# Optimization experiments

Measured on AMD Instinct MI355X. Metric: run time of the kernel, lower is better.

## Reference

```python
import jax, jax.numpy as jnp
import numpy as np

N_NODES = 20000
N_EDGES = 320000
H = 4        # heads
C = 64       # channels per head
D = H * C    # 256, also input_dim
L = 4        # num_layers
NEG_SLOPE = 0.2


def setup_inputs() -> dict:
    key = jax.random.key(0)
    ks = jax.random.split(key, 8)
    x = jax.random.normal(ks[0], (N_NODES, D), jnp.float32)
    edge_index = jax.random.randint(ks[1], (2, N_EDGES), 0, N_NODES, dtype=jnp.int64)
    Ws = jax.random.normal(ks[2], (L, D, D), jnp.float32) * 0.05
    att_src = jax.random.normal(ks[3], (L, H, C), jnp.float32) * 0.05
    att_dst = jax.random.normal(ks[4], (L, H, C), jnp.float32) * 0.05
    biases = jax.random.normal(ks[5], (L, D), jnp.float32) * 0.05
    Wout = jax.random.normal(ks[6], (D, D), jnp.float32) * 0.05
    bout = jax.random.normal(ks[7], (D,), jnp.float32) * 0.05
    return {"x": x, "edge_index": edge_index, "Ws": Ws, "att_src": att_src,
            "att_dst": att_dst, "biases": biases, "Wout": Wout, "bout": bout}


def reference(x, edge_index, Ws, att_src, att_dst, biases, Wout, bout):
    n = x.shape[0]
    # PyG GATConv adds self-loops by default; same edge set each layer.
    loops = jnp.arange(n, dtype=edge_index.dtype)
    src = jnp.concatenate([edge_index[0], loops])  # message sources
    dst = jnp.concatenate([edge_index[1], loops])  # message targets (softmax groups)
    h = x
    for l in range(L):
        hp = (h @ Ws[l]).reshape(n, H, C)                      # [N,H,C]
        a_s = jnp.einsum('nhc,hc->nh', hp, att_src[l])          # [N,H]
        a_d = jnp.einsum('nhc,hc->nh', hp, att_dst[l])          # [N,H]
        e = jax.nn.leaky_relu(a_s[src] + a_d[dst], NEG_SLOPE)   # [E',H]
        # per-destination segment softmax (every node has a self-loop -> non-empty)
        m = jax.ops.segment_max(e, dst, num_segments=n)         # [N,H]
        ex = jnp.exp(e - m[dst])
        denom = jax.ops.segment_sum(ex, dst, num_segments=n)    # [N,H]
        alpha = ex / denom[dst]                                 # [E',H]
        msg = hp[src] * alpha[:, :, None]                       # [E',H,C]
        h = jax.ops.segment_sum(msg, dst, num_segments=n).reshape(n, D) + biases[l]
        h = jax.nn.elu(h)  # dropout is identity in eval mode
    g = jnp.mean(h, axis=0, keepdims=True)                      # mean pooling, single graph
    return g @ Wout + bout                                      # [1, D]
```

## Files before the change

### kernel.cpp

```cpp
#include <hip/hip_runtime.h>
#include <hip/hip_bf16.h>

#define H 4
#define C 64
#define D 256
#define NEG_SLOPE 0.2f
#define ESHIFT 8.0f

typedef _Float16 half_t;
typedef __attribute__((ext_vector_type(8))) _Float16 half8v;
typedef __attribute__((ext_vector_type(4))) float f32x4;


__device__ inline void fma_mix_pair(float& clo, float& chi, unsigned wu, float a) {
    asm("v_fma_mix_f32 %0, %2, %3, %0 op_sel_hi:[1,0,0]\n\t"
        "v_fma_mix_f32 %1, %2, %3, %1 op_sel:[1,0,0] op_sel_hi:[1,0,0]"
        : "+v"(clo), "+v"(chi)
        : "v"(wu), "v"(a));
}

__global__ void count_kernel(const int* __restrict__ ei, int E, int N, int* __restrict__ counts) {
    int i = blockIdx.x * blockDim.x + threadIdx.x;
    if (i >= E + N) return;
    int d = (i < E) ? ei[E + i] : (i - E);
    atomicAdd(&counts[d], 1);
}

__global__ __launch_bounds__(1024) void scan1(const int* __restrict__ counts,
                                              int* __restrict__ row_ptr,
                                              int* __restrict__ bsum, int N) {
    __shared__ int wsum[16];
    int tid = threadIdx.x, lane = tid & 63, wid = tid >> 6;
    int idx = blockIdx.x * 1024 + tid;
    int v = (idx < N) ? counts[idx] : 0;
    int val = v;
    #pragma unroll
    for (int o = 1; o < 64; o <<= 1) {
        int t = __shfl_up(val, o);
        if (lane >= o) val += t;
    }
    if (lane == 63) wsum[wid] = val;
    __syncthreads();
    int woff = 0;
    #pragma unroll
    for (int w = 0; w < 16; w++) woff += (w < wid) ? wsum[w] : 0;
    if (idx < N) row_ptr[idx] = woff + val - v;
    if (tid == 1023) bsum[blockIdx.x] = woff + val;
}

__global__ void scan2(int* __restrict__ bsum, int* __restrict__ row_ptr, int nb, int N) {
    int lane = threadIdx.x;
    int v = (lane < nb) ? bsum[lane] : 0;
    int val = v;
    #pragma unroll
    for (int o = 1; o < 64; o <<= 1) {
        int t = __shfl_up(val, o);
        if (lane >= o) val += t;
    }
    if (lane < nb) bsum[lane] = val - v;
    if (lane == 63) row_ptr[N] = val;
}

__global__ __launch_bounds__(1024) void scan3(int* __restrict__ row_ptr,
                                              const int* __restrict__ bsum,
                                              int* __restrict__ cursor, int N) {
    int idx = blockIdx.x * 1024 + threadIdx.x;
    if (idx >= N) return;
    int r = row_ptr[idx] + bsum[blockIdx.x];
    row_ptr[idx] = r;
    cursor[idx] = r;
}

__global__ void scatter_kernel(const int* __restrict__ ei, int E, int N,
                               int* __restrict__ cursor, int* __restrict__ csr_src) {
    int i = blockIdx.x * blockDim.x + threadIdx.x;
    if (i >= E + N) return;
    int s, d;
    if (i < E) { s = ei[i]; d = ei[E + i]; }
    else       { s = d = i - E; }
    int pos = atomicAdd(&cursor[d], 1);
    csr_src[pos] = s;
}

__global__ void conv_x(const float* __restrict__ in, half_t* __restrict__ xt, int total) {
    int t = blockIdx.x * blockDim.x + threadIdx.x;
    if (t >= total) return;
    int i = t >> 5, o = t & 31;
    const float* src = in + (size_t)i * 256 + o * 8;
    float4 v0 = *(const float4*)src;
    float4 v1 = *(const float4*)(src + 4);
    half_t q[8] __attribute__((aligned(16)));
    q[0] = (half_t)v0.x; q[1] = (half_t)v0.y; q[2] = (half_t)v0.z; q[3] = (half_t)v0.w;
    q[4] = (half_t)v1.x; q[5] = (half_t)v1.y; q[6] = (half_t)v1.z; q[7] = (half_t)v1.w;
    size_t dst = (size_t)(i >> 4) * 4096 + (o >> 2) * 512 + (o & 3) * 128 + (i & 15) * 8;
    *(half8v*)(xt + dst) = *(half8v*)q;
}

__global__ void conv_w(const float* __restrict__ W, half_t* __restrict__ wt, int total) {
    int idx = blockIdx.x * blockDim.x + threadIdx.x;
    if (idx >= total) return;
    int Lr = idx & 63;
    int s  = (idx >> 6) & 7;
    int cb = (idx >> 9) & 3;
    int h  = (idx >> 11) & 3;
    int l  = idx >> 13;
    int col = h * 64 + cb * 16 + (Lr & 15);
    int k0  = 32 * s + (Lr >> 4) * 8;
    half_t q[8] __attribute__((aligned(16)));
    #pragma unroll
    for (int j = 0; j < 8; j++)
        q[j] = (half_t)W[(size_t)l * 65536 + (size_t)(k0 + j) * 256 + col];
    *(half8v*)(wt + (size_t)idx * 8) = *(half8v*)q;
}

__global__ __launch_bounds__(256) void gemm_f16(
    const half_t* __restrict__ At, const half_t* __restrict__ Wt,
    const float* __restrict__ asrc, const float* __restrict__ adst,
    half_t* __restrict__ hp, float* __restrict__ as_out, float* __restrict__ ad_out,
    int Npad) {
    __shared__ float sp[2][4][16], sd[2][4][16];
    int cb = threadIdx.x >> 6, lane = threadIdx.x & 63;
    int h = blockIdx.x & 3, pg = blockIdx.x >> 2;
    int rlo = lane & 15, q = lane >> 4;
    const half_t* pb = Wt + (size_t)h * 16384 + (size_t)cb * 4096 + lane * 8;

    half8v B[8];
    #pragma unroll
    for (int s = 0; s < 8; s++) B[s] = *(const half8v*)(pb + s * 512);

    float av = asrc[h * 64 + cb * 16 + rlo];
    float dv = adst[h * 64 + cb * 16 + rlo];
    half_t* hph = hp + (size_t)h * Npad * 64;

    #pragma unroll
    for (int pp = 0; pp < 4; pp++) {
        int p = pg * 4 + pp;
        const half_t* pa = At + (size_t)p * 4096 + lane * 8;

        f32x4 acc = (f32x4){0.f, 0.f, 0.f, 0.f};
        half8v A0 = *(const half8v*)(pa);
        half8v A1;
        #pragma unroll
        for (int s = 0; s < 8; s += 2) {
            A1 = *(const half8v*)(pa + (s + 1) * 512);
            acc = __builtin_amdgcn_mfma_f32_16x16x32_f16(A0, B[s], acc, 0, 0, 0);
            if (s < 6) A0 = *(const half8v*)(pa + (s + 2) * 512);
            acc = __builtin_amdgcn_mfma_f32_16x16x32_f16(A1, B[s + 1], acc, 0, 0, 0);
        }

        int grow = p * 16 + q * 4;
        #pragma unroll
        for (int i = 0; i < 4; i++)
            hph[(size_t)(grow + i) * 64 + cb * 16 + rlo] = (half_t)acc[i];

        float ps[4], pd[4];
        #pragma unroll
        for (int i = 0; i < 4; i++) { ps[i] = acc[i] * av; pd[i] = acc[i] * dv; }
        #pragma unroll
        for (int mask = 1; mask <= 8; mask <<= 1) {
            #pragma unroll
            for (int i = 0; i < 4; i++) {
                ps[i] += __shfl_xor(ps[i], mask);
                pd[i] += __shfl_xor(pd[i], mask);
            }
        }
        int par = pp & 1;
        if (rlo == 0) {
            #pragma unroll
            for (int i = 0; i < 4; i++) {
                sp[par][cb][q * 4 + i] = ps[i];
                sd[par][cb][q * 4 + i] = pd[i];
            }
        }
        __syncthreads();
        if (threadIdx.x < 16) {
            int r = threadIdx.x;
            float s_ = sp[par][0][r] + sp[par][1][r] + sp[par][2][r] + sp[par][3][r];
            float d_ = sd[par][0][r] + sd[par][1][r] + sd[par][2][r] + sd[par][3][r];
            as_out[(size_t)(p * 16 + r) * 4 + h] = s_;
            ad_out[(size_t)(p * 16 + r) * 4 + h] = d_;
        }
    }
}

#define AGG_BODY(g)                                                          \
    {                                                                        \
        int e_ = 2 * (g) + es;                                               \
        int s_ = __float_as_int(pk[wv][e_][0]);                              \
        float a_ = pk[wv][e_][4 + hh];                                       \
        const uint4 w_ = *(const uint4*)(hpb + (size_t)s_ * 64);             \
        asum += a_;                                                          \
        fma_mix_pair(c0, c1, w_.x, a_);                                      \
        fma_mix_pair(c2, c3, w_.y, a_);                                      \
        fma_mix_pair(c4, c5, w_.z, a_);                                      \
        fma_mix_pair(c6, c7, w_.w, a_);                                      \
    }

__global__ __launch_bounds__(256) void gat_aggregate(
    const half_t* __restrict__ hp, const float* __restrict__ as_, const float* __restrict__ ad_,
    const int* __restrict__ row_ptr, const int* __restrict__ csr_src,
    const float* __restrict__ bias, half_t* __restrict__ hnext, int N, int Npad) {
    __shared__ float pk[4][64][8];
    int wv = threadIdx.x >> 6, lane = threadIdx.x & 63;
    int d = blockIdx.x * 4 + wv;
    if (d >= N) return;
    int r0 = row_ptr[d], deg = row_ptr[d + 1] - r0;
    float4 adv = *(const float4*)&ad_[(size_t)d * 4];

    if (deg <= 64) {
        if (lane < deg) {
            int s = csr_src[r0 + lane];
            float4 as4 = *(const float4*)&as_[(size_t)s * 4];
            float e0 = as4.x + adv.x, e1 = as4.y + adv.y;
            float e2 = as4.z + adv.z, e3 = as4.w + adv.w;
            e0 = e0 > 0.f ? e0 : NEG_SLOPE * e0;
            e1 = e1 > 0.f ? e1 : NEG_SLOPE * e1;
            e2 = e2 > 0.f ? e2 : NEG_SLOPE * e2;
            e3 = e3 > 0.f ? e3 : NEG_SLOPE * e3;
            float4 ex;
            ex.x = __expf(e0 - ESHIFT);
            ex.y = __expf(e1 - ESHIFT);
            ex.z = __expf(e2 - ESHIFT);
            ex.w = __expf(e3 - ESHIFT);
            pk[wv][lane][0] = __int_as_float(s);
            *(float4*)&pk[wv][lane][4] = ex;
        }

        int hh = lane >> 4;
        int es = (lane >> 3) & 1;
        int chq = lane & 7;
        const half_t* hpb = hp + (size_t)hh * Npad * 64 + chq * 8;
        float c0 = 0.f, c1 = 0.f, c2 = 0.f, c3 = 0.f;
        float c4 = 0.f, c5 = 0.f, c6 = 0.f, c7 = 0.f;
        float asum = 0.f;
        int full = deg >> 1;
        int g = 0;
        for (; g + 4 <= full; g += 4) {
            AGG_BODY(g) AGG_BODY(g + 1) AGG_BODY(g + 2) AGG_BODY(g + 3)
        }
        for (; g < full; g++) { AGG_BODY(g) }
        if ((deg & 1) && es == 0) {
            int e_ = deg - 1;
            int s_ = __float_as_int(pk[wv][e_][0]);
            float a_ = pk[wv][e_][4 + hh];
            const uint4 w_ = *(const uint4*)(hpb + (size_t)s_ * 64);
            asum += a_;
            fma_mix_pair(c0, c1, w_.x, a_);
            fma_mix_pair(c2, c3, w_.y, a_);
            fma_mix_pair(c4, c5, w_.z, a_);
            fma_mix_pair(c6, c7, w_.w, a_);
        }
        c0 += __shfl_xor(c0, 8); c1 += __shfl_xor(c1, 8);
        c2 += __shfl_xor(c2, 8); c3 += __shfl_xor(c3, 8);
        c4 += __shfl_xor(c4, 8); c5 += __shfl_xor(c5, 8);
        c6 += __shfl_xor(c6, 8); c7 += __shfl_xor(c7, 8);
        asum += __shfl_xor(asum, 8);
        if (!(lane & 8)) {
            float inv = 1.0f / asum;
            int o = hh * 8 + chq;
            const float* bp = bias + o * 8;
            float vv[8] = {c0, c1, c2, c3, c4, c5, c6, c7};
            half_t oh[8] __attribute__((aligned(16)));
            #pragma unroll
            for (int j = 0; j < 8; j++) {
                float v = vv[j] * inv + bp[j];
                v = v > 0.f ? v : (__expf(v) - 1.0f);
                oh[j] = (half_t)v;
            }
            size_t dst = (size_t)(d >> 4) * 4096 + (o >> 2) * 512 + (o & 3) * 128 + (d & 15) * 8;
            *(half8v*)(hnext + dst) = *(half8v*)oh;
        }
    } else {
        float advA[4] = {adv.x, adv.y, adv.z, adv.w};
        #pragma unroll
        for (int hh = 0; hh < 4; hh++) {
            float advh = advA[hh];
            float ssum = 0.f;
            for (int i = lane; i < deg; i += 64) {
                int s = csr_src[r0 + i];
                float e = as_[(size_t)s * 4 + hh] + advh;
                e = e > 0.f ? e : NEG_SLOPE * e;
                ssum += __expf(e - ESHIFT);
            }
            #pragma unroll
            for (int o = 32; o; o >>= 1) ssum += __shfl_xor(ssum, o);
            float inv = 1.0f / ssum;
            const half_t* hph = hp + (size_t)hh * Npad * 64;
            float acc = 0.f;
            for (int i = 0; i < deg; i++) {
                int s = csr_src[r0 + i];
                float e = as_[(size_t)s * 4 + hh] + advh;
                e = e > 0.f ? e : NEG_SLOPE * e;
                acc += __expf(e - ESHIFT) * (float)hph[(size_t)s * 64 + lane];
            }
            float v = acc * inv + bias[hh * 64 + lane];
            v = v > 0.f ? v : (__expf(v) - 1.0f);
            int c = hh * 64 + lane;
            size_t dst = (size_t)(d >> 4) * 4096 + (c >> 5) * 512 + ((c >> 3) & 3) * 128 + (d & 15) * 8 + (c & 7);
            hnext[dst] = (half_t)v;
        }
    }
}

__global__ __launch_bounds__(256) void col_sum_f16(const half_t* __restrict__ hin,
                                                   float* __restrict__ partial, int N, int rows_per_blk) {
    int c = threadIdx.x;
    int r0 = blockIdx.x * rows_per_blk;
    int r1 = min(r0 + rows_per_blk, N);
    int coff = (c >> 5) * 512 + ((c >> 3) & 3) * 128 + (c & 7);
    float acc = 0.f;
    for (int r = r0; r < r1; r++)
        acc += (float)hin[(size_t)(r >> 4) * 4096 + coff + (r & 15) * 8];
    partial[(size_t)blockIdx.x * 256 + c] = acc;
}

__global__ __launch_bounds__(256) void final_kernel(const float* __restrict__ partial,
                                                    const float* __restrict__ Wout,
                                                    const float* __restrict__ bout,
                                                    float* __restrict__ out, float invN, int nb) {
    __shared__ float gl[256];
    int j = threadIdx.x;
    float s = 0.f;
    for (int b = 0; b < nb; b++) s += partial[(size_t)b * 256 + j];
    gl[j] = s;
    __syncthreads();
    float acc = 0.f;
    for (int i = 0; i < 256; i++) acc += gl[i] * Wout[i * 256 + j];
    out[j] = acc * invN + bout[j];
}

extern "C" void kernel_launch(void* const* d_in, const int* in_sizes, int n_in,
                              void* d_out, int out_size, void* d_ws, size_t ws_size,
                              hipStream_t stream) {
    const float* x       = (const float*)d_in[0];
    const int*   ei      = (const int*)d_in[1];
    const float* Ws      = (const float*)d_in[2];
    const float* att_src = (const float*)d_in[3];
    const float* att_dst = (const float*)d_in[4];
    const float* biases  = (const float*)d_in[5];
    const float* Wout    = (const float*)d_in[6];
    const float* bout    = (const float*)d_in[7];
    float* out = (float*)d_out;

    int N = in_sizes[0] / D;
    int E = in_sizes[1] / 2;
    int L = in_sizes[2] / (D * D);
    int Etot = E + N;
    int Npad = (N + 63) & ~63;

    char* ws = (char*)d_ws;
    size_t off = 0;
    auto alloc = [&](size_t bytes) -> void* {
        void* p = ws + off;
        off = (off + bytes + 255) & ~(size_t)255;
        return p;
    };
    half_t* xt     = (half_t*)alloc((size_t)Npad * D * 2);
    half_t* hp     = (half_t*)alloc((size_t)Npad * D * 2);
    float* a_s     = (float*)alloc((size_t)Npad * H * 4);
    float* a_d     = (float*)alloc((size_t)Npad * H * 4);
    half_t* wt     = (half_t*)alloc((size_t)L * D * D * 2);
    int*   counts  = (int*)alloc((size_t)N * 4);
    int*   row_ptr = (int*)alloc((size_t)(N + 1) * 4);
    int*   cursor  = (int*)alloc((size_t)N * 4);
    int*   bsum    = (int*)alloc(64 * 4);
    int*   csr_src = (int*)alloc((size_t)Etot * 4);
    int rows_per_blk = 254;
    int nb_pool = (N + rows_per_blk - 1) / rows_per_blk;
    float* partial = (float*)alloc((size_t)nb_pool * 256 * 4);
    if (off > ws_size) return;

    int thr = 256;

    int xtot = N * 32;
    conv_x<<<(xtot + thr - 1) / thr, thr, 0, stream>>>(x, xt, xtot);
    int wtot = L * 4 * 4 * 8 * 64;
    conv_w<<<(wtot + thr - 1) / thr, thr, 0, stream>>>(Ws, wt, wtot);

    hipMemsetAsync(counts, 0, (size_t)N * 4, stream);
    count_kernel<<<(Etot + thr - 1) / thr, thr, 0, stream>>>(ei, E, N, counts);
    int nb_scan = (N + 1023) / 1024;
    scan1<<<nb_scan, 1024, 0, stream>>>(counts, row_ptr, bsum, N);
    scan2<<<1, 64, 0, stream>>>(bsum, row_ptr, nb_scan, N);
    scan3<<<nb_scan, 1024, 0, stream>>>(row_ptr, bsum, cursor, N);
    scatter_kernel<<<(Etot + thr - 1) / thr, thr, 0, stream>>>(ei, E, N, cursor, csr_src);

    int gemm_blocks = (Npad / 64) * 4;
    int agg_blocks = (N + 3) / 4;
    for (int l = 0; l < L; l++) {
        gemm_f16<<<gemm_blocks, 256, 0, stream>>>(
            xt, wt + (size_t)l * D * D,
            att_src + (size_t)l * H * C, att_dst + (size_t)l * H * C,
            hp, a_s, a_d, Npad);
        gat_aggregate<<<agg_blocks, 256, 0, stream>>>(
            hp, a_s, a_d, row_ptr, csr_src, biases + (size_t)l * D, xt, N, Npad);
    }

    col_sum_f16<<<nb_pool, thr, 0, stream>>>(xt, partial, N, rows_per_blk);
    final_kernel<<<1, thr, 0, stream>>>(partial, Wout, bout, out, 1.0f / (float)N, nb_pool);
}
```

Before: 269.4 us.

## Precompute edge attention weights per head and split aggregation by head

Adds a separate per-edge kernel that computes the exponentiated leaky-relu attention scores for all four heads into a head-major array, using a new CSR destination array. The aggregation kernel is restructured so each block handles one head. A wave now processes 8 edges in parallel for a single head instead of 2 edges across 4 heads, and reduces the partial sums with shuffles and an LDS transpose. This moves the exp and attention gathers out of the aggregation and aims at better gather locality per head. The cost is an extra kernel launch, an extra edge-sized array write and read per layer, and four times as many aggregation blocks that each re-read the CSR indices.

```diff
diff --git a/kernel.cpp b/kernel.cpp
--- a/kernel.cpp
+++ b/kernel.cpp
@@ -72,7 +72,8 @@
 }
 
 __global__ void scatter_kernel(const int* __restrict__ ei, int E, int N,
-                               int* __restrict__ cursor, int* __restrict__ csr_src) {
+                               int* __restrict__ cursor,
+                               int* __restrict__ csr_src, int* __restrict__ csr_dst) {
     int i = blockIdx.x * blockDim.x + threadIdx.x;
     if (i >= E + N) return;
     int s, d;
@@ -80,6 +81,7 @@
     else       { s = d = i - E; }
     int pos = atomicAdd(&cursor[d], 1);
     csr_src[pos] = s;
+    csr_dst[pos] = d;
 }
 
 __global__ void conv_x(const float* __restrict__ in, half_t* __restrict__ xt, int total) {
@@ -183,11 +185,32 @@
     }
 }
 
+__global__ __launch_bounds__(256) void alpha_kernel(
+    const float* __restrict__ a_s, const float* __restrict__ a_d,
+    const int* __restrict__ csr_src, const int* __restrict__ csr_dst,
+    float* __restrict__ alpha, int Etot) {
+    int j = blockIdx.x * blockDim.x + threadIdx.x;
+    if (j >= Etot) return;
+    int s = csr_src[j], d = csr_dst[j];
+    float4 as4 = *(const float4*)&a_s[(size_t)s * 4];
+    float4 ad4 = *(const float4*)&a_d[(size_t)d * 4];
+    float e0 = as4.x + ad4.x, e1 = as4.y + ad4.y;
+    float e2 = as4.z + ad4.z, e3 = as4.w + ad4.w;
+    e0 = e0 > 0.f ? e0 : NEG_SLOPE * e0;
+    e1 = e1 > 0.f ? e1 : NEG_SLOPE * e1;
+    e2 = e2 > 0.f ? e2 : NEG_SLOPE * e2;
+    e3 = e3 > 0.f ? e3 : NEG_SLOPE * e3;
+    alpha[j]            = __expf(e0 - ESHIFT);
+    alpha[Etot + j]     = __expf(e1 - ESHIFT);
+    alpha[2 * Etot + j] = __expf(e2 - ESHIFT);
+    alpha[3 * Etot + j] = __expf(e3 - ESHIFT);
+}
+
 #define AGG_BODY(g)                                                          \
     {                                                                        \
-        int e_ = 2 * (g) + es;                                               \
+        int e_ = (g) * 8 + es;                                               \
         int s_ = __float_as_int(pk[wv][e_][0]);                              \
-        float a_ = pk[wv][e_][4 + hh];                                       \
+        float a_ = pk[wv][e_][1];                                            \
         const uint4 w_ = *(const uint4*)(hpb + (size_t)s_ * 64);             \
         asum += a_;                                                          \
         fma_mix_pair(c0, c1, w_.x, a_);                                      \
@@ -197,108 +220,89 @@
     }
 
 __global__ __launch_bounds__(256) void gat_aggregate(
-    const half_t* __restrict__ hp, const float* __restrict__ as_, const float* __restrict__ ad_,
+    const half_t* __restrict__ hp, const float* __restrict__ alpha,
     const int* __restrict__ row_ptr, const int* __restrict__ csr_src,
-    const float* __restrict__ bias, half_t* __restrict__ hnext, int N, int Npad) {
-    __shared__ float pk[4][64][8];
+    const float* __restrict__ bias, half_t* __restrict__ hnext,
+    int N, int Npad, int ngroups, int Etot) {
+    __shared__ float pk[4][64][2];
+    __shared__ half_t lds_o[4][64];
     int wv = threadIdx.x >> 6, lane = threadIdx.x & 63;
-    int d = blockIdx.x * 4 + wv;
+    int h = blockIdx.x / ngroups;
+    int d = (blockIdx.x % ngroups) * 4 + wv;
     if (d >= N) return;
     int r0 = row_ptr[d], deg = row_ptr[d + 1] - r0;
-    float4 adv = *(const float4*)&ad_[(size_t)d * 4];
+    const float* alh = alpha + (size_t)h * Etot;
+    const half_t* hph = hp + (size_t)h * Npad * 64;
 
     if (deg <= 64) {
         if (lane < deg) {
-            int s = csr_src[r0 + lane];
-            float4 as4 = *(const float4*)&as_[(size_t)s * 4];
-            float e0 = as4.x + adv.x, e1 = as4.y + adv.y;
-            float e2 = as4.z + adv.z, e3 = as4.w + adv.w;
-            e0 = e0 > 0.f ? e0 : NEG_SLOPE * e0;
-            e1 = e1 > 0.f ? e1 : NEG_SLOPE * e1;
-            e2 = e2 > 0.f ? e2 : NEG_SLOPE * e2;
-            e3 = e3 > 0.f ? e3 : NEG_SLOPE * e3;
-            float4 ex;
-            ex.x = __expf(e0 - ESHIFT);
-            ex.y = __expf(e1 - ESHIFT);
-            ex.z = __expf(e2 - ESHIFT);
-            ex.w = __expf(e3 - ESHIFT);
-            pk[wv][lane][0] = __int_as_float(s);
-            *(float4*)&pk[wv][lane][4] = ex;
-        }
-
-        int hh = lane >> 4;
-        int es = (lane >> 3) & 1;
-        int chq = lane & 7;
-        const half_t* hpb = hp + (size_t)hh * Npad * 64 + chq * 8;
+            pk[wv][lane][0] = __int_as_float(csr_src[r0 + lane]);
+            pk[wv][lane][1] = alh[r0 + lane];
+        }
+        int es = lane >> 3, chq = lane & 7;
+        const half_t* hpb = hph + chq * 8;
         float c0 = 0.f, c1 = 0.f, c2 = 0.f, c3 = 0.f;
         float c4 = 0.f, c5 = 0.f, c6 = 0.f, c7 = 0.f;
         float asum = 0.f;
-        int full = deg >> 1;
+        int full = deg >> 3;
         int g = 0;
-        for (; g + 4 <= full; g += 4) {
-            AGG_BODY(g) AGG_BODY(g + 1) AGG_BODY(g + 2) AGG_BODY(g + 3)
-        }
+        for (; g + 2 <= full; g += 2) { AGG_BODY(g) AGG_BODY(g + 1) }
         for (; g < full; g++) { AGG_BODY(g) }
-        if ((deg & 1) && es == 0) {
-            int e_ = deg - 1;
-            int s_ = __float_as_int(pk[wv][e_][0]);
-            float a_ = pk[wv][e_][4 + hh];
-            const uint4 w_ = *(const uint4*)(hpb + (size_t)s_ * 64);
-            asum += a_;
-            fma_mix_pair(c0, c1, w_.x, a_);
-            fma_mix_pair(c2, c3, w_.y, a_);
-            fma_mix_pair(c4, c5, w_.z, a_);
-            fma_mix_pair(c6, c7, w_.w, a_);
-        }
-        c0 += __shfl_xor(c0, 8); c1 += __shfl_xor(c1, 8);
-        c2 += __shfl_xor(c2, 8); c3 += __shfl_xor(c3, 8);
-        c4 += __shfl_xor(c4, 8); c5 += __shfl_xor(c5, 8);
-        c6 += __shfl_xor(c6, 8); c7 += __shfl_xor(c7, 8);
-        asum += __shfl_xor(asum, 8);
-        if (!(lane & 8)) {
-            float inv = 1.0f / asum;
-            int o = hh * 8 + chq;
-            const float* bp = bias + o * 8;
-            float vv[8] = {c0, c1, c2, c3, c4, c5, c6, c7};
-            half_t oh[8] __attribute__((aligned(16)));
-            #pragma unroll
-            for (int j = 0; j < 8; j++) {
-                float v = vv[j] * inv + bp[j];
-                v = v > 0.f ? v : (__expf(v) - 1.0f);
-                oh[j] = (half_t)v;
+        {
+            int e0 = full * 8 + es;
+            if (e0 < deg) {
+                int s_ = __float_as_int(pk[wv][e0][0]);
+                float a_ = pk[wv][e0][1];
+                const uint4 w_ = *(const uint4*)(hpb + (size_t)s_ * 64);
+                asum += a_;
+                fma_mix_pair(c0, c1, w_.x, a_);
+                fma_mix_pair(c2, c3, w_.y, a_);
+                fma_mix_pair(c4, c5, w_.z, a_);
+                fma_mix_pair(c6, c7, w_.w, a_);
             }
+        }
+        #pragma unroll
+        for (int o = 8; o <= 32; o <<= 1) {
+            c0 += __shfl_xor(c0, o); c1 += __shfl_xor(c1, o);
+            c2 += __shfl_xor(c2, o); c3 += __shfl_xor(c3, o);
+            c4 += __shfl_xor(c4, o); c5 += __shfl_xor(c5, o);
+            c6 += __shfl_xor(c6, o); c7 += __shfl_xor(c7, o);
+            asum += __shfl_xor(asum, o);
+        }
+        float inv = 1.0f / asum;
+        float t0 = (es & 1) ? c1 : c0;
+        float t1 = (es & 1) ? c3 : c2;
+        float t2 = (es & 1) ? c5 : c4;
+        float t3 = (es & 1) ? c7 : c6;
+        float u0 = (es & 2) ? t1 : t0;
+        float u1 = (es & 2) ? t3 : t2;
+        float v  = (es & 4) ? u1 : u0;
+        int ch = chq * 8 + es;
+        v = v * inv + bias[h * 64 + ch];
+        v = v > 0.f ? v : (__expf(v) - 1.0f);
+        lds_o[wv][ch] = (half_t)v;
+        if (es == 0) {
+            half8v ov = *(half8v*)&lds_o[wv][chq * 8];
+            int o = h * 8 + chq;
             size_t dst = (size_t)(d >> 4) * 4096 + (o >> 2) * 512 + (o & 3) * 128 + (d & 15) * 8;
-            *(half8v*)(hnext + dst) = *(half8v*)oh;
+            *(half8v*)(hnext + dst) = ov;
         }
     } else {
-        float advA[4] = {adv.x, adv.y, adv.z, adv.w};
-        #pragma unroll
-        for (int hh = 0; hh < 4; hh++) {
-            float advh = advA[hh];
-            float ssum = 0.f;
-            for (int i = lane; i < deg; i += 64) {
-                int s = csr_src[r0 + i];
-                float e = as_[(size_t)s * 4 + hh] + advh;
-                e = e > 0.f ? e : NEG_SLOPE * e;
-                ssum += __expf(e - ESHIFT);
-            }
-            #pragma unroll
-            for (int o = 32; o; o >>= 1) ssum += __shfl_xor(ssum, o);
-            float inv = 1.0f / ssum;
-            const half_t* hph = hp + (size_t)hh * Npad * 64;
-            float acc = 0.f;
-            for (int i = 0; i < deg; i++) {
-                int s = csr_src[r0 + i];
-                float e = as_[(size_t)s * 4 + hh] + advh;
-                e = e > 0.f ? e : NEG_SLOPE * e;
-                acc += __expf(e - ESHIFT) * (float)hph[(size_t)s * 64 + lane];
-            }
-            float v = acc * inv + bias[hh * 64 + lane];
-            v = v > 0.f ? v : (__expf(v) - 1.0f);
-            int c = hh * 64 + lane;
-            size_t dst = (size_t)(d >> 4) * 4096 + (c >> 5) * 512 + ((c >> 3) & 3) * 128 + (d & 15) * 8 + (c & 7);
-            hnext[dst] = (half_t)v;
-        }
+        float ssum = 0.f;
+        for (int i = lane; i < deg; i += 64) ssum += alh[r0 + i];
+        #pragma unroll
+        for (int o = 32; o; o >>= 1) ssum += __shfl_xor(ssum, o);
+        float inv = 1.0f / ssum;
+        float acc = 0.f;
+        for (int i = 0; i < deg; i++) {
+            int s = csr_src[r0 + i];
+            acc += alh[r0 + i] * (float)hph[(size_t)s * 64 + lane];
+        }
+        float v = acc * inv + bias[h * 64 + lane];
+        v = v > 0.f ? v : (__expf(v) - 1.0f);
+        int c = h * 64 + lane;
+        size_t dst = (size_t)(d >> 4) * 4096 + (c >> 5) * 512 + ((c >> 3) & 3) * 128 + (d & 15) * 8 + (c & 7);
+        hnext[dst] = (half_t)v;
     }
 }
 
@@ -360,11 +364,13 @@
     float* a_s     = (float*)alloc((size_t)Npad * H * 4);
     float* a_d     = (float*)alloc((size_t)Npad * H * 4);
     half_t* wt     = (half_t*)alloc((size_t)L * D * D * 2);
+    float* alpha   = (float*)alloc((size_t)H * Etot * 4);
     int*   counts  = (int*)alloc((size_t)N * 4);
     int*   row_ptr = (int*)alloc((size_t)(N + 1) * 4);
     int*   cursor  = (int*)alloc((size_t)N * 4);
     int*   bsum    = (int*)alloc(64 * 4);
     int*   csr_src = (int*)alloc((size_t)Etot * 4);
+    int*   csr_dst = (int*)alloc((size_t)Etot * 4);
     int rows_per_blk = 254;
     int nb_pool = (N + rows_per_blk - 1) / rows_per_blk;
     float* partial = (float*)alloc((size_t)nb_pool * 256 * 4);
@@ -383,17 +389,20 @@
     scan1<<<nb_scan, 1024, 0, stream>>>(counts, row_ptr, bsum, N);
     scan2<<<1, 64, 0, stream>>>(bsum, row_ptr, nb_scan, N);
     scan3<<<nb_scan, 1024, 0, stream>>>(row_ptr, bsum, cursor, N);
-    scatter_kernel<<<(Etot + thr - 1) / thr, thr, 0, stream>>>(ei, E, N, cursor, csr_src);
+    scatter_kernel<<<(Etot + thr - 1) / thr, thr, 0, stream>>>(ei, E, N, cursor, csr_src, csr_dst);
 
     int gemm_blocks = (Npad / 64) * 4;
-    int agg_blocks = (N + 3) / 4;
+    int ngroups = (N + 3) / 4;
+    int agg_blocks = 4 * ngroups;
     for (int l = 0; l < L; l++) {
         gemm_f16<<<gemm_blocks, 256, 0, stream>>>(
             xt, wt + (size_t)l * D * D,
             att_src + (size_t)l * H * C, att_dst + (size_t)l * H * C,
             hp, a_s, a_d, Npad);
+        alpha_kernel<<<(Etot + thr - 1) / thr, thr, 0, stream>>>(
+            a_s, a_d, csr_src, csr_dst, alpha, Etot);
         gat_aggregate<<<agg_blocks, 256, 0, stream>>>(
-            hp, a_s, a_d, row_ptr, csr_src, biases + (size_t)l * D, xt, N, Npad);
+            hp, alpha, row_ptr, csr_src, biases + (size_t)l * D, xt, N, Npad, ngroups, Etot);
     }
 
     col_sum_f16<<<nb_pool, thr, 0, stream>>>(xt, partial, N, rows_per_blk);
```

After: 323.0 us. 1.2x slower.
